# Kernel tuning notes

Hardware: AMD Instinct MI355X
Metric: run time of the kernel (lower is better)

The kernel has to match this reference:

```python
import jax, jax.numpy as jnp
import numpy as np

SIGMA = 7.0
KERNEL_SIZE = int(2 * np.ceil(SIGMA * 2) + 1)  # 29
PAD = (KERNEL_SIZE - 1) // 2  # 14


def _gaussian_kernel2d():
    variance = SIGMA ** 2
    coords = jnp.arange(KERNEL_SIZE, dtype=jnp.float32)
    mean = (KERNEL_SIZE - 1) / 2.0
    xg, yg = jnp.meshgrid(coords, coords, indexing='xy')
    k = jnp.exp(-((xg - mean) ** 2 + (yg - mean) ** 2) / (2.0 * variance))
    k = k / (2.0 * np.pi * variance)
    return k / k.sum()  # [K, K]


def setup_inputs() -> dict:
    key = jax.random.key(0)
    x = jax.random.normal(key, (8, 64, 256, 256), dtype=jnp.float32)
    return {"x": x}


def reference(x):
    channels = x.shape[1]
    k2d = _gaussian_kernel2d().astype(x.dtype)
    # depthwise weights: [C, 1, K, K] (OIHW with feature_group_count=C)
    w = jnp.broadcast_to(k2d, (channels, 1, KERNEL_SIZE, KERNEL_SIZE))
    xp = jnp.pad(x, ((0, 0), (0, 0), (PAD, PAD), (PAD, PAD)), mode='reflect')
    out = jax.lax.conv_general_dilated(
        xp, w,
        window_strides=(1, 1),
        padding='VALID',
        dimension_numbers=('NCHW', 'OIHW', 'NCHW'),
        feature_group_count=channels,
    )
    return out
```

## Files before the change

kernel.cpp:

```cpp
#include <hip/hip_runtime.h>

#define IMG   256
#define TILE  64
#define KS    29
#define PAD   14
#define LDSS  100

static constexpr float GK[15] = {
    1.0f,        0.98984780f, 0.96000544f, 0.91225408f, 0.84936581f,
    0.77483743f, 0.69256933f, 0.60653066f, 0.52045012f, 0.43756474f,
    0.36044779f, 0.29092381f, 0.23006630f, 0.17826398f, 0.13533528f
};
static constexpr float GSUM =
    GK[0] + 2.0f * (GK[1] + GK[2] + GK[3] + GK[4] + GK[5] + GK[6] + GK[7] +
                    GK[8] + GK[9] + GK[10] + GK[11] + GK[12] + GK[13] + GK[14]);
static constexpr float WT[29] = {
    GK[14]/GSUM, GK[13]/GSUM, GK[12]/GSUM, GK[11]/GSUM, GK[10]/GSUM, GK[9]/GSUM, GK[8]/GSUM,
    GK[7]/GSUM,  GK[6]/GSUM,  GK[5]/GSUM,  GK[4]/GSUM,  GK[3]/GSUM,  GK[2]/GSUM, GK[1]/GSUM,
    GK[0]/GSUM,
    GK[1]/GSUM,  GK[2]/GSUM,  GK[3]/GSUM,  GK[4]/GSUM,  GK[5]/GSUM,  GK[6]/GSUM, GK[7]/GSUM,
    GK[8]/GSUM,  GK[9]/GSUM,  GK[10]/GSUM, GK[11]/GSUM, GK[12]/GSUM, GK[13]/GSUM, GK[14]/GSUM
};

__device__ __forceinline__ int refl(int p) {
    int a = p < 0 ? -p : p;
    int b = 510 - a;
    return a < b ? a : b;
}

__global__ __launch_bounds__(384, 8)
void gauss_sep2(const float* __restrict__ x, float* __restrict__ out) {
    __shared__ alignas(16) float s_tmp[TILE * LDSS];

    const int t   = threadIdx.x;
    const int img = blockIdx.z;
    const int y0  = blockIdx.y * TILE;
    const int x0  = blockIdx.x * TILE;

    const float* __restrict__ src = x   + (size_t)img * (IMG * IMG);
    float* __restrict__ dst       = out + (size_t)img * (IMG * IMG);

    {
        const int yg = t / 96;
        const int xp = t - yg * 96;
        if (xp < 92) {
            const int gx   = refl(x0 + xp - PAD);
            const int brow = y0 + yg * 16 - PAD;
            float acc[16];
            #pragma unroll
            for (int j = 0; j < 16; ++j) acc[j] = 0.f;
            #pragma unroll
            for (int s = 0; s < 16 + KS - 1; ++s) {
                const int rr  = refl(brow + s);
                const float v = src[rr * IMG + gx];
                #pragma unroll
                for (int j = 0; j < 16; ++j) {
                    const int k = s - j;
                    if (k >= 0 && k < KS) acc[j] += WT[k] * v;
                }
            }
            #pragma unroll
            for (int j = 0; j < 16; ++j)
                s_tmp[(yg * 16 + j) * LDSS + xp] = acc[j];
        }
    }
    __syncthreads();

    {
        const int y  = t & 63;
        const int cg = t >> 6;
        if (cg < 4) {
            const int c0 = cg * 16;
            float acc[16];
            #pragma unroll
            for (int c = 0; c < 16; ++c) acc[c] = 0.f;
            const float4* srow = (const float4*)&s_tmp[y * LDSS + c0];
            #pragma unroll
            for (int m = 0; m < 11; ++m) {
                const float4 v4 = srow[m];
                #pragma unroll
                for (int q = 0; q < 4; ++q) {
                    const int p = 4 * m + q;
                    const float v = q == 0 ? v4.x : q == 1 ? v4.y : q == 2 ? v4.z : v4.w;
                    #pragma unroll
                    for (int c = 0; c < 16; ++c) {
                        const int k = p - c;
                        if (k >= 0 && k < KS) acc[c] += WT[k] * v;
                    }
                }
            }
            float4* orow = (float4*)&dst[(size_t)(y0 + y) * IMG + x0 + c0];
            #pragma unroll
            for (int m = 0; m < 4; ++m)
                orow[m] = make_float4(acc[4*m+0], acc[4*m+1], acc[4*m+2], acc[4*m+3]);
        }
    }
}

extern "C" void kernel_launch(void* const* d_in, const int* in_sizes, int n_in,
                              void* d_out, int out_size, void* d_ws, size_t ws_size,
                              hipStream_t stream) {
    const float* x = (const float*)d_in[0];
    float* out = (float*)d_out;
    const int images = in_sizes[0] / (IMG * IMG);
    dim3 grid(IMG / TILE, IMG / TILE, images);
    gauss_sep2<<<grid, dim3(384), 0, stream>>>(x, out);
}
```

Measured before the change: 97.90 us.

## Process full-width row strips to remove horizontal halo recomputation

Replaces the 64x64 tiles with full-width 64-row strips of 1024 threads. Each thread computes the vertical pass for one full column, and the horizontal reflection padding is built in LDS by mirroring edge columns, so the horizontal halo is no longer reloaded or recomputed. A fast path skips the reflect index math for interior rows. In exchange, the larger LDS footprint (about 72KB) and 1024-thread blocks reduce occupancy and give fewer blocks per image.

```diff
diff --git a/kernel.cpp b/kernel.cpp
--- a/kernel.cpp
+++ b/kernel.cpp
@@ -1,10 +1,10 @@
 #include <hip/hip_runtime.h>
 
 #define IMG   256
-#define TILE  64
+#define TILEY 64
 #define KS    29
 #define PAD   14
-#define LDSS  100
+#define LDSS  284
 
 static constexpr float GK[15] = {
     1.0f,        0.98984780f, 0.96000544f, 0.91225408f, 0.84936581f,
@@ -24,76 +24,99 @@
 
 __device__ __forceinline__ int refl(int p) {
     int a = p < 0 ? -p : p;
-    int b = 510 - a;
+    int b = 2 * (IMG - 1) - a;
     return a < b ? a : b;
 }
 
-__global__ __launch_bounds__(384, 8)
-void gauss_sep2(const float* __restrict__ x, float* __restrict__ out) {
-    __shared__ alignas(16) float s_tmp[TILE * LDSS];
+__global__ __launch_bounds__(1024, 8)
+void gauss_strip(const float* __restrict__ x, float* __restrict__ out) {
+    __shared__ alignas(16) float s[TILEY * LDSS];
 
     const int t   = threadIdx.x;
-    const int img = blockIdx.z;
-    const int y0  = blockIdx.y * TILE;
-    const int x0  = blockIdx.x * TILE;
+    const int img = blockIdx.y;
+    const int y0  = blockIdx.x * TILEY;
 
     const float* __restrict__ src = x   + (size_t)img * (IMG * IMG);
-    float* __restrict__ dst       = out + (size_t)img * (IMG * IMG);
+    float*       __restrict__ dst = out + (size_t)img * (IMG * IMG);
 
     {
-        const int yg = t / 96;
-        const int xp = t - yg * 96;
-        if (xp < 92) {
-            const int gx   = refl(x0 + xp - PAD);
-            const int brow = y0 + yg * 16 - PAD;
-            float acc[16];
+        const int col  = t & 255;
+        const int rg   = t >> 8;
+        const int r0   = rg * 16;
+        const int brow = y0 + r0 - PAD;
+
+        float acc[16];
+        #pragma unroll
+        for (int j = 0; j < 16; ++j) acc[j] = 0.f;
+
+        if (brow >= 0 && brow + 43 <= IMG - 1) {
+            const float* p = src + (size_t)brow * IMG + col;
             #pragma unroll
-            for (int j = 0; j < 16; ++j) acc[j] = 0.f;
-            #pragma unroll
-            for (int s = 0; s < 16 + KS - 1; ++s) {
-                const int rr  = refl(brow + s);
-                const float v = src[rr * IMG + gx];
+            for (int sidx = 0; sidx < 16 + KS - 1; ++sidx) {
+                const float v = p[sidx * IMG];
                 #pragma unroll
                 for (int j = 0; j < 16; ++j) {
-                    const int k = s - j;
+                    const int k = sidx - j;
                     if (k >= 0 && k < KS) acc[j] += WT[k] * v;
                 }
             }
+        } else {
+            #pragma unroll
+            for (int sidx = 0; sidx < 16 + KS - 1; ++sidx) {
+                const float v = src[refl(brow + sidx) * IMG + col];
+                #pragma unroll
+                for (int j = 0; j < 16; ++j) {
+                    const int k = sidx - j;
+                    if (k >= 0 && k < KS) acc[j] += WT[k] * v;
+                }
+            }
+        }
+
+        const int pos = PAD + col;
+        #pragma unroll
+        for (int j = 0; j < 16; ++j)
+            s[(r0 + j) * LDSS + pos] = acc[j];
+        if (col >= 1 && col <= PAD) {
             #pragma unroll
             for (int j = 0; j < 16; ++j)
-                s_tmp[(yg * 16 + j) * LDSS + xp] = acc[j];
+                s[(r0 + j) * LDSS + (PAD - col)] = acc[j];
+        } else if (col >= IMG - 1 - PAD && col <= IMG - 2) {
+            #pragma unroll
+            for (int j = 0; j < 16; ++j)
+                s[(r0 + j) * LDSS + (2 * (IMG - 1) + PAD - col)] = acc[j];
         }
     }
     __syncthreads();
 
     {
-        const int y  = t & 63;
-        const int cg = t >> 6;
-        if (cg < 4) {
-            const int c0 = cg * 16;
-            float acc[16];
+        const int row = t & 63;
+        const int cg  = t >> 6;
+        const int c0  = cg * 16;
+
+        float acc[16];
+        #pragma unroll
+        for (int c = 0; c < 16; ++c) acc[c] = 0.f;
+
+        const float4* srow = (const float4*)&s[row * LDSS + c0];
+        #pragma unroll
+        for (int m = 0; m < 11; ++m) {
+            const float4 v4 = srow[m];
             #pragma unroll
-            for (int c = 0; c < 16; ++c) acc[c] = 0.f;
-            const float4* srow = (const float4*)&s_tmp[y * LDSS + c0];
-            #pragma unroll
-            for (int m = 0; m < 11; ++m) {
-                const float4 v4 = srow[m];
+            for (int q = 0; q < 4; ++q) {
+                const int p = 4 * m + q;
+                const float v = q == 0 ? v4.x : q == 1 ? v4.y : q == 2 ? v4.z : v4.w;
                 #pragma unroll
-                for (int q = 0; q < 4; ++q) {
-                    const int p = 4 * m + q;
-                    const float v = q == 0 ? v4.x : q == 1 ? v4.y : q == 2 ? v4.z : v4.w;
-                    #pragma unroll
-                    for (int c = 0; c < 16; ++c) {
-                        const int k = p - c;
-                        if (k >= 0 && k < KS) acc[c] += WT[k] * v;
-                    }
+                for (int c = 0; c < 16; ++c) {
+                    const int k = p - c;
+                    if (k >= 0 && k < KS) acc[c] += WT[k] * v;
                 }
             }
-            float4* orow = (float4*)&dst[(size_t)(y0 + y) * IMG + x0 + c0];
-            #pragma unroll
-            for (int m = 0; m < 4; ++m)
-                orow[m] = make_float4(acc[4*m+0], acc[4*m+1], acc[4*m+2], acc[4*m+3]);
         }
+
+        float4* orow = (float4*)&dst[(size_t)(y0 + row) * IMG + c0];
+        #pragma unroll
+        for (int m = 0; m < 4; ++m)
+            orow[m] = make_float4(acc[4*m+0], acc[4*m+1], acc[4*m+2], acc[4*m+3]);
     }
 }
 
@@ -103,6 +126,6 @@
     const float* x = (const float*)d_in[0];
     float* out = (float*)d_out;
     const int images = in_sizes[0] / (IMG * IMG);
-    dim3 grid(IMG / TILE, IMG / TILE, images);
-    gauss_sep2<<<grid, dim3(384), 0, stream>>>(x, out);
+    dim3 grid(IMG / TILEY, images);
+    gauss_strip<<<grid, dim3(1024), 0, stream>>>(x, out);
 }
```

Measured after the change: 80.94 us. 1.21x faster.

## Tile full-width row strips with fp16 LDS staging and in-LDS horizontal reflection

Applied to the files above, without the earlier changes.

Each block now handles a 32-row by full-width strip. It loads the 60 needed input rows with coalesced float4 reads and stores them as fp16 in shared memory. The vertical pass runs from LDS, and reflection padding for the horizontal pass is written into LDS instead of recomputed per load. This is meant to cut redundant global reads and the gather-style column loads of the tiled version. The cost is fp16 rounding of inputs, which lowers accuracy, and heavy LDS use per block, which limits occupancy.

```diff
diff --git a/kernel.cpp b/kernel.cpp
--- a/kernel.cpp
+++ b/kernel.cpp
@@ -1,10 +1,13 @@
 #include <hip/hip_runtime.h>
+#include <hip/hip_fp16.h>
 
 #define IMG   256
-#define TILE  64
+#define SROWS 32
+#define RAWR  60
 #define KS    29
 #define PAD   14
-#define LDSS  100
+#define LDSS  292
+#define MOFF  16
 
 static constexpr float GK[15] = {
     1.0f,        0.98984780f, 0.96000544f, 0.91225408f, 0.84936581f,
@@ -24,76 +27,120 @@
 
 __device__ __forceinline__ int refl(int p) {
     int a = p < 0 ? -p : p;
-    int b = 510 - a;
+    int b = 2 * (IMG - 1) - a;
     return a < b ? a : b;
 }
 
-__global__ __launch_bounds__(384, 8)
-void gauss_sep2(const float* __restrict__ x, float* __restrict__ out) {
-    __shared__ alignas(16) float s_tmp[TILE * LDSS];
+__global__ __launch_bounds__(512, 4)
+void gauss_v11(const float* __restrict__ x, float* __restrict__ out) {
+    __shared__ __half raw[RAWR * 256];
+    __shared__ float  tmp[SROWS * LDSS];
 
     const int t   = threadIdx.x;
-    const int img = blockIdx.z;
-    const int y0  = blockIdx.y * TILE;
-    const int x0  = blockIdx.x * TILE;
+    const int img = blockIdx.y;
+    const int y0  = blockIdx.x * SROWS;
 
     const float* __restrict__ src = x   + (size_t)img * (IMG * IMG);
-    float* __restrict__ dst       = out + (size_t)img * (IMG * IMG);
+    float*       __restrict__ dst = out + (size_t)img * (IMG * IMG);
 
-    {
-        const int yg = t / 96;
-        const int xp = t - yg * 96;
-        if (xp < 92) {
-            const int gx   = refl(x0 + xp - PAD);
-            const int brow = y0 + yg * 16 - PAD;
-            float acc[16];
-            #pragma unroll
-            for (int j = 0; j < 16; ++j) acc[j] = 0.f;
-            #pragma unroll
-            for (int s = 0; s < 16 + KS - 1; ++s) {
-                const int rr  = refl(brow + s);
-                const float v = src[rr * IMG + gx];
-                #pragma unroll
-                for (int j = 0; j < 16; ++j) {
-                    const int k = s - j;
-                    if (k >= 0 && k < KS) acc[j] += WT[k] * v;
-                }
-            }
-            #pragma unroll
-            for (int j = 0; j < 16; ++j)
-                s_tmp[(yg * 16 + j) * LDSS + xp] = acc[j];
+    #pragma unroll
+    for (int k = 0; k < 8; ++k) {
+        const int i = t + k * 512;
+        if (i < RAWR * 64) {
+            const int r  = i >> 6;
+            const int c4 = (i & 63) << 2;
+            const int gr = refl(y0 - PAD + r);
+            const float4 v = *(const float4*)(src + (size_t)gr * IMG + c4);
+            __half2 a = __float22half2_rn(make_float2(v.x, v.y));
+            __half2 b = __float22half2_rn(make_float2(v.z, v.w));
+            uint2 pk;
+            pk.x = *(unsigned int*)&a;
+            pk.y = *(unsigned int*)&b;
+            *(uint2*)&raw[r * 256 + c4] = pk;
         }
     }
     __syncthreads();
 
     {
-        const int y  = t & 63;
-        const int cg = t >> 6;
-        if (cg < 4) {
-            const int c0 = cg * 16;
-            float acc[16];
+        const int cp = t & 127;
+        const int rg = t >> 7;
+        const int r0 = rg * 8;
+
+        float2 acc[8];
+        #pragma unroll
+        for (int j = 0; j < 8; ++j) acc[j] = make_float2(0.f, 0.f);
+
+        #pragma unroll
+        for (int s = 0; s < 36; ++s) {
+            const __half2 h = *(__half2*)&raw[(r0 + s) * 256 + 2 * cp];
+            const float2 v = __half22float2(h);
             #pragma unroll
-            for (int c = 0; c < 16; ++c) acc[c] = 0.f;
-            const float4* srow = (const float4*)&s_tmp[y * LDSS + c0];
-            #pragma unroll
-            for (int m = 0; m < 11; ++m) {
-                const float4 v4 = srow[m];
-                #pragma unroll
-                for (int q = 0; q < 4; ++q) {
-                    const int p = 4 * m + q;
-                    const float v = q == 0 ? v4.x : q == 1 ? v4.y : q == 2 ? v4.z : v4.w;
-                    #pragma unroll
-                    for (int c = 0; c < 16; ++c) {
-                        const int k = p - c;
-                        if (k >= 0 && k < KS) acc[c] += WT[k] * v;
-                    }
+            for (int j = 0; j < 8; ++j) {
+                const int k = s - j;
+                if (k >= 0 && k < KS) {
+                    acc[j].x += WT[k] * v.x;
+                    acc[j].y += WT[k] * v.y;
                 }
             }
-            float4* orow = (float4*)&dst[(size_t)(y0 + y) * IMG + x0 + c0];
+        }
+
+        #pragma unroll
+        for (int j = 0; j < 8; ++j)
+            *(float2*)&tmp[(r0 + j) * LDSS + MOFF + 2 * cp] = acc[j];
+
+        if (cp <= 7) {
             #pragma unroll
-            for (int m = 0; m < 4; ++m)
-                orow[m] = make_float4(acc[4*m+0], acc[4*m+1], acc[4*m+2], acc[4*m+3]);
+            for (int q = 0; q < 2; ++q) {
+                const int c = 2 * cp + q;
+                if (c >= 1 && c <= PAD) {
+                    #pragma unroll
+                    for (int j = 0; j < 8; ++j)
+                        tmp[(r0 + j) * LDSS + (MOFF - c)] = q == 0 ? acc[j].x : acc[j].y;
+                }
+            }
+        } else if (cp >= 120) {
+            #pragma unroll
+            for (int q = 0; q < 2; ++q) {
+                const int c = 2 * cp + q;
+                if (c >= IMG - 1 - PAD && c <= IMG - 2) {
+                    #pragma unroll
+                    for (int j = 0; j < 8; ++j)
+                        tmp[(r0 + j) * LDSS + (MOFF + 2 * (IMG - 1) - c)] = q == 0 ? acc[j].x : acc[j].y;
+                }
+            }
         }
+    }
+    __syncthreads();
+
+    {
+        const int row = t & 31;
+        const int cg  = t >> 5;
+        const int c0b = cg * 16;
+
+        float acc[16];
+        #pragma unroll
+        for (int c = 0; c < 16; ++c) acc[c] = 0.f;
+
+        const float4* w = (const float4*)&tmp[row * LDSS + c0b];
+        #pragma unroll
+        for (int m = 0; m < 12; ++m) {
+            const float4 v4 = w[m];
+            #pragma unroll
+            for (int q = 0; q < 4; ++q) {
+                const int e = 4 * m + q;
+                const float val = q == 0 ? v4.x : q == 1 ? v4.y : q == 2 ? v4.z : v4.w;
+                #pragma unroll
+                for (int c = 0; c < 16; ++c) {
+                    const int k = e - 2 - c;
+                    if (k >= 0 && k < KS) acc[c] += WT[k] * val;
+                }
+            }
+        }
+
+        float4* orow = (float4*)&dst[(size_t)(y0 + row) * IMG + c0b];
+        #pragma unroll
+        for (int m = 0; m < 4; ++m)
+            orow[m] = make_float4(acc[4*m+0], acc[4*m+1], acc[4*m+2], acc[4*m+3]);
     }
 }
 
@@ -103,6 +150,6 @@
     const float* x = (const float*)d_in[0];
     float* out = (float*)d_out;
     const int images = in_sizes[0] / (IMG * IMG);
-    dim3 grid(IMG / TILE, IMG / TILE, images);
-    gauss_sep2<<<grid, dim3(384), 0, stream>>>(x, out);
+    dim3 grid(IMG / SROWS, images);
+    gauss_v11<<<grid, dim3(512), 0, stream>>>(x, out);
 }
```

After: 97.79 us. About the same (-0.1%).
